# Performance work log

Hardware: AMD Instinct MI355X
Metric: run time of the kernel (lower is better)

## Reference

```python
import jax, jax.numpy as jnp
import numpy as np

NUM_HEADS = 12


def setup_inputs() -> dict:
    key = jax.random.key(0)
    ks = jax.random.split(key, 6)
    B, N, C = 16, 576, 768
    H, D = NUM_HEADS, 768 // NUM_HEADS
    P = 16
    x = jax.random.normal(ks[0], (B, N, C), dtype=jnp.float32)
    prompt = jax.random.normal(ks[1], (B, 2, P, H, D), dtype=jnp.float32)
    act_scale = jax.random.uniform(ks[2], (2,), dtype=jnp.float32)
    qkv_w = jax.random.normal(ks[3], (3 * C, C), dtype=jnp.float32) * (C ** -0.5)
    proj_w = jax.random.normal(ks[4], (C, C), dtype=jnp.float32) * (C ** -0.5)
    proj_b = jnp.zeros((C,), dtype=jnp.float32)
    return {"x": x, "prompt": prompt, "act_scale": act_scale,
            "qkv_w": qkv_w, "proj_w": proj_w, "proj_b": proj_b}


def reference(x, prompt, act_scale, qkv_w, proj_w, proj_b):
    B, N, C = x.shape
    H = NUM_HEADS
    D = C // H
    scale = D ** -0.5
    # qkv projection: [B,N,3C] -> (3,B,H,N,D)
    qkv = (x @ qkv_w.T).reshape(B, N, 3, H, D).transpose(2, 0, 3, 1, 4)
    q, k, v = qkv[0], qkv[1], qkv[2]
    # prompt: [B,2,P,H,D] -> (2,B,H,P,D)
    pr = jnp.transpose(prompt, (1, 0, 3, 2, 4))
    key_prefix, value_prefix = pr[0], pr[1]        # [B,H,P,D]
    v = jnp.concatenate([value_prefix, v], axis=2)  # [B,H,P+N,D]
    # gated prefix scores
    prompt_attn = jnp.einsum('bhnd,bhpd->bhnp', q, key_prefix) * scale
    prompt_attn = prompt_attn + jnp.tanh(prompt_attn * act_scale[0]) * act_scale[1]
    # standard scores
    attn = jnp.einsum('bhnd,bhmd->bhnm', q, k) * scale
    attn = jnp.concatenate([prompt_attn, attn], axis=-1)  # [B,H,N,P+N]
    attn = jax.nn.softmax(attn, axis=-1)
    out = jnp.einsum('bhnm,bhmd->bhnd', attn, v)  # [B,H,N,D]
    out = out.transpose(0, 2, 1, 3).reshape(B, N, C)
    return out @ proj_w.T + proj_b
```

## Files before the change

kernel.cpp:

```cpp
#include <hip/hip_runtime.h>
#include <hip/hip_bf16.h>
#include <math.h>

namespace {

constexpr int kB = 16, kN = 576, kC = 768, kH = 12, kP = 16;
constexpr int kM = kB * kN;

typedef __attribute__((ext_vector_type(8))) __bf16 bf16x8;
typedef __attribute__((ext_vector_type(4))) float  f32x4;
typedef __attribute__((ext_vector_type(8))) unsigned short u16x8;

__device__ inline unsigned short f2bf(float f) {
  __bf16 h = (__bf16)f;
  return __builtin_bit_cast(unsigned short, h);
}
__device__ inline float bf2f(unsigned short u) {
  unsigned int x = ((unsigned int)u) << 16;
  return __builtin_bit_cast(float, x);
}
__device__ inline unsigned int pk2bf(float lo, float hi) {
  return (unsigned int)f2bf(lo) | ((unsigned int)f2bf(hi) << 16);
}
__device__ inline int xcd_swz(int hw, int nwg) {
  const int per = nwg >> 3;
  return (hw & 7) * per + (hw >> 3);
}

#define GLDS16(src, dst) __builtin_amdgcn_global_load_lds( \
    (const __attribute__((address_space(1))) unsigned int*)(src), \
    (__attribute__((address_space(3))) unsigned int*)(dst), 16, 0, 0)

__global__ __launch_bounds__(256)
void cvt3(const float* __restrict__ x, const float* __restrict__ wq,
          const float* __restrict__ wp, unsigned short* __restrict__ xo,
          unsigned short* __restrict__ wqo, unsigned short* __restrict__ wpo) {
  const int bid = blockIdx.x;
  const float* in; unsigned short* out; int base;
  if (bid < 6912)       { in = x;  out = xo;  base = bid; }
  else if (bid < 8640)  { in = wq; out = wqo; base = bid - 6912; }
  else                  { in = wp; out = wpo; base = bid - 8640; }
  const int i = base * 256 + threadIdx.x;
  const float4 v = ((const float4*)in)[i];
  ((ushort4*)out)[i] = make_ushort4(f2bf(v.x), f2bf(v.y), f2bf(v.z), f2bf(v.w));
}

template<int OB>
__global__ __launch_bounds__(256)
void gemm_bf16(const unsigned short* __restrict__ A, const unsigned short* __restrict__ W,
               const float* __restrict__ bias, void* __restrict__ Yv, int Kd, int Nd) {
  __shared__ __align__(16) unsigned short As[2][4096];
  __shared__ __align__(16) unsigned short Bs[2][4096];
  const int tid  = threadIdx.x;
  const int wv   = tid >> 6, lane = tid & 63;
  const int gx   = Nd >> 7;
  const int lg   = xcd_swz(blockIdx.x, gridDim.x);
  const long bm  = (long)(lg / gx) * 128;
  const long bn  = (long)(lg % gx) * 128;
  const int wr   = (wv >> 1) * 64;
  const int wc   = (wv & 1) * 64;
  const int row15 = lane & 15, kg = lane >> 4;

  auto stage = [&](int buf, int kt) {
#pragma unroll
    for (int site = 0; site < 2; ++site) {
      const int p = site * 256 + tid;
      const int row = p >> 2, slot = (p & 3) ^ (row & 3);
      const unsigned short* srcA = A + (bm + row) * (long)Kd + kt + slot * 8;
      const unsigned short* srcB = W + (bn + row) * (long)Kd + kt + slot * 8;
      GLDS16(srcA, &As[buf][site * 2048 + wv * 512]);
      GLDS16(srcB, &Bs[buf][site * 2048 + wv * 512]);
    }
  };

  f32x4 acc[4][4] = {};
  stage(0, 0);
  __syncthreads();

  const int swg = row15 & 3;
  const int nt = Kd >> 5;
  for (int t = 0; t < nt; ++t) {
    const int cur = t & 1;
    if (t + 1 < nt) stage(cur ^ 1, (t + 1) << 5);

    bf16x8 af[4], bf_[4];
#pragma unroll
    for (int mi = 0; mi < 4; ++mi)
      af[mi] = *(const bf16x8*)(&As[cur][(wr + mi * 16 + row15) * 32 + ((kg ^ swg) << 3)]);
#pragma unroll
    for (int ni = 0; ni < 4; ++ni)
      bf_[ni] = *(const bf16x8*)(&Bs[cur][(wc + ni * 16 + row15) * 32 + ((kg ^ swg) << 3)]);
#pragma unroll
    for (int mi = 0; mi < 4; ++mi)
#pragma unroll
      for (int ni = 0; ni < 4; ++ni)
        acc[mi][ni] = __builtin_amdgcn_mfma_f32_16x16x32_bf16(af[mi], bf_[ni], acc[mi][ni], 0, 0, 0);
    __syncthreads();
  }

  const int r4 = kg * 4;
#pragma unroll
  for (int ni = 0; ni < 4; ++ni) {
    const long col = bn + wc + ni * 16 + row15;
    if constexpr (OB) {
      unsigned short* Y = (unsigned short*)Yv;
#pragma unroll
      for (int mi = 0; mi < 4; ++mi)
#pragma unroll
        for (int j = 0; j < 4; ++j)
          Y[(bm + wr + mi * 16 + r4 + j) * (long)Nd + col] = f2bf(acc[mi][ni][j]);
    } else {
      float* Y = (float*)Yv;
      const float bv = bias ? bias[col] : 0.0f;
#pragma unroll
      for (int mi = 0; mi < 4; ++mi)
#pragma unroll
        for (int j = 0; j < 4; ++j)
          Y[(bm + wr + mi * 16 + r4 + j) * (long)Nd + col] = acc[mi][ni][j] + bv;
    }
  }
}

__device__ inline void softmax_group_static(f32x4 (&c)[4], float& lsum,
                                            unsigned short* pl,
                                            const int kg, const int sw) {
  float psum = 0.0f;
#pragma unroll
  for (int kb = 0; kb < 4; ++kb) {
    const float p0 = __expf(c[kb][0] - 10.0f);
    const float p1 = __expf(c[kb][1] - 10.0f);
    const float p2 = __expf(c[kb][2] - 10.0f);
    const float p3 = __expf(c[kb][3] - 10.0f);
    psum += (p0 + p1) + (p2 + p3);
    const int off = (((kb * 2 + (kg >> 1)) ^ sw) << 3) + (kg & 1) * 4;
    *(uint2*)(pl + off) = make_uint2(pk2bf(p0, p1), pk2bf(p2, p3));
  }
  lsum += psum;
}

__global__ __launch_bounds__(192, 3)
void attn_mfma(const unsigned short* __restrict__ qkv, const float* __restrict__ prompt,
               const float* __restrict__ act_scale, unsigned short* __restrict__ attn_out) {
  const int lg = xcd_swz(blockIdx.x, gridDim.x);
  const int qt = lg % 6, bh = lg / 6;
  const int h = bh % kH, b = bh / kH;
  const int tid = threadIdx.x, wv = tid >> 6, lane = tid & 63;
  const int q15 = lane & 15, kg = lane >> 4;

  __shared__ __align__(16) unsigned short Klds[2][4096];
  __shared__ __align__(16) unsigned short Vt[2][4096];
  __shared__ __align__(16) unsigned short Plds[3][2048];

  const float a0 = act_scale[0], a1 = act_scale[1];
  const int sw  = q15 & 7;
  const int sl0 = (kg ^ sw) << 3;
  const int sl1 = ((4 + kg) ^ sw) << 3;

  bf16x8 qf[2][2];
#pragma unroll
  for (int g = 0; g < 2; ++g) {
    const unsigned short* qrow =
        qkv + (size_t)(b * kN + qt * 96 + wv * 32 + g * 16 + q15) * 2304 + h * 64;
#pragma unroll
    for (int dh = 0; dh < 2; ++dh) {
      u16x8 raw = *(const u16x8*)(qrow + dh * 32 + kg * 8);
      u16x8 sc;
#pragma unroll
      for (int j = 0; j < 8; ++j) sc[j] = f2bf(bf2f(raw[j]) * 0.125f);
      qf[g][dh] = __builtin_bit_cast(bf16x8, sc);
    }
  }

  if (tid < 128) {
    const int r = tid >> 3, s = tid & 7;
    const float* src = prompt + (((size_t)(b * 2) * kP + r) * kH + h) * 64 + s * 8;
    const f32x4 f0 = *(const f32x4*)src, f1 = *(const f32x4*)(src + 4);
    *(uint4*)(&Klds[0][r * 64 + ((s ^ (r & 7)) << 3)]) =
        make_uint4(pk2bf(f0[0], f0[1]), pk2bf(f0[2], f0[3]),
                   pk2bf(f1[0], f1[1]), pk2bf(f1[2], f1[3]));
  }
  if (tid < 128) {
    const int kp = tid & 7, vdq = tid >> 3;
    const float* s0 = prompt + (((size_t)(b * 2 + 1) * kP + 2 * kp) * kH + h) * 64 + vdq * 4;
    const f32x4 x0 = *(const f32x4*)s0;
    const f32x4 y0 = *(const f32x4*)(s0 + kH * 64);
#pragma unroll
    for (int j = 0; j < 4; ++j) {
      const int d = vdq * 4 + j;
      *(unsigned int*)(&Vt[0][d * 64 + (((kp >> 2) ^ (d & 7)) << 3) + (kp & 3) * 2]) =
          pk2bf(x0[j], y0[j]);
    }
  }
#pragma unroll
  for (int i = 0; i < 2; ++i) {
    const int idx = tid + 192 * i;
    const int d = idx / 6, szl = (idx % 6) + 2;
    *(uint4*)(&Vt[0][d * 64 + ((szl ^ (d & 7)) << 3)]) = make_uint4(0, 0, 0, 0);
  }
  __syncthreads();

  f32x4 o0[4] = {}, o1[4] = {};
  float l0 = 0.0f, l1 = 0.0f;

  const int vkp  = tid & 31;
  const int vdgb = tid >> 5;
  const int kr8  = lane >> 3, ks8 = lane & 7;

  for (int ch = 0; ch < 10; ++ch) {
    const int cur = ch & 1;

    u16x8 va0, va1, vb0, vb1;
    const bool doV = (ch < 9) && (wv < 2);
    if (ch < 9) {
      if (doV) {
        const unsigned short* r0 = qkv + (size_t)(b * kN + ch * 64 + 2 * vkp) * 2304 + 1536 + h * 64;
        va0 = *(const u16x8*)(r0 + vdgb * 8);
        va1 = *(const u16x8*)(r0 + (vdgb + 4) * 8);
        vb0 = *(const u16x8*)(r0 + 2304 + vdgb * 8);
        vb1 = *(const u16x8*)(r0 + 2304 + (vdgb + 4) * 8);
      } else if (wv == 2) {
#pragma unroll
        for (int g8 = 0; g8 < 8; ++g8) {
          const int r = g8 * 8 + kr8;
          const unsigned short* src =
              qkv + (size_t)(b * kN + ch * 64 + r) * 2304 + 768 + h * 64 + ((ks8 ^ (r & 7)) << 3);
          GLDS16(src, &Klds[cur ^ 1][g8 * 512]);
        }
      }
    }

    f32x4 c0[4], c1[4];
    __builtin_amdgcn_s_setprio(1);
#pragma unroll
    for (int kb = 0; kb < 4; ++kb) {
      if (ch == 0 && kb > 0) {
        c0[kb][0] = c0[kb][1] = c0[kb][2] = c0[kb][3] = -1.0e30f;
        c1[kb][0] = c1[kb][1] = c1[kb][2] = c1[kb][3] = -1.0e30f;
      } else {
        const unsigned short* krow = &Klds[cur][(kb * 16 + q15) * 64];
        const bf16x8 k0 = *(const bf16x8*)(krow + sl0);
        const bf16x8 k1 = *(const bf16x8*)(krow + sl1);
        f32x4 t0 = {}, t1 = {};
        t0 = __builtin_amdgcn_mfma_f32_16x16x32_bf16(k0, qf[0][0], t0, 0, 0, 0);
        c0[kb] = __builtin_amdgcn_mfma_f32_16x16x32_bf16(k1, qf[0][1], t0, 0, 0, 0);
        t1 = __builtin_amdgcn_mfma_f32_16x16x32_bf16(k0, qf[1][0], t1, 0, 0, 0);
        c1[kb] = __builtin_amdgcn_mfma_f32_16x16x32_bf16(k1, qf[1][1], t1, 0, 0, 0);
      }
    }
    __builtin_amdgcn_s_setprio(0);
    if (ch == 0) {
#pragma unroll
      for (int j = 0; j < 4; ++j) {
        const float s0v = c0[0][j];
        const float e0 = __expf(2.0f * s0v * a0);
        c0[0][j] = s0v + ((e0 - 1.0f) / (e0 + 1.0f)) * a1;
        const float s1v = c1[0][j];
        const float e1 = __expf(2.0f * s1v * a0);
        c1[0][j] = s1v + ((e1 - 1.0f) / (e1 + 1.0f)) * a1;
      }
    }

    softmax_group_static(c0, l0, &Plds[wv][q15 * 64], kg, sw);
    softmax_group_static(c1, l1, &Plds[wv][(q15 + 16) * 64], kg, sw);

    if (doV) {
#pragma unroll
      for (int j = 0; j < 8; ++j) {
        const int d0 = vdgb * 8 + j;
        *(unsigned int*)(&Vt[cur ^ 1][d0 * 64 + (((vkp >> 2) ^ (d0 & 7)) << 3) + (vkp & 3) * 2]) =
            (unsigned int)va0[j] | ((unsigned int)vb0[j] << 16);
        const int d1 = (vdgb + 4) * 8 + j;
        *(unsigned int*)(&Vt[cur ^ 1][d1 * 64 + (((vkp >> 2) ^ (d1 & 7)) << 3) + (vkp & 3) * 2]) =
            (unsigned int)va1[j] | ((unsigned int)vb1[j] << 16);
      }
    }

    const unsigned short* p0 = &Plds[wv][q15 * 64];
    const unsigned short* p1 = &Plds[wv][(q15 + 16) * 64];
    const bf16x8 pa00 = *(const bf16x8*)(p0 + sl0);
    const bf16x8 pa01 = *(const bf16x8*)(p0 + sl1);
    const bf16x8 pa10 = *(const bf16x8*)(p1 + sl0);
    const bf16x8 pa11 = *(const bf16x8*)(p1 + sl1);
    __builtin_amdgcn_s_setprio(1);
#pragma unroll
    for (int nb = 0; nb < 4; ++nb) {
      const unsigned short* vr = &Vt[cur][(nb * 16 + q15) * 64];
      const bf16x8 bv0 = *(const bf16x8*)(vr + sl0);
      const bf16x8 bv1 = *(const bf16x8*)(vr + sl1);
      o0[nb] = __builtin_amdgcn_mfma_f32_16x16x32_bf16(pa00, bv0, o0[nb], 0, 0, 0);
      o0[nb] = __builtin_amdgcn_mfma_f32_16x16x32_bf16(pa01, bv1, o0[nb], 0, 0, 0);
      o1[nb] = __builtin_amdgcn_mfma_f32_16x16x32_bf16(pa10, bv0, o1[nb], 0, 0, 0);
      o1[nb] = __builtin_amdgcn_mfma_f32_16x16x32_bf16(pa11, bv1, o1[nb], 0, 0, 0);
    }
    __builtin_amdgcn_s_setprio(0);

    __syncthreads();
  }

  l0 += __shfl_xor(l0, 16, 64);
  l0 += __shfl_xor(l0, 32, 64);
  l1 += __shfl_xor(l1, 16, 64);
  l1 += __shfl_xor(l1, 32, 64);
  const float i0 = 1.0f / l0, i1 = 1.0f / l1;
  float iq0[4], iq1[4];
#pragma unroll
  for (int jr = 0; jr < 4; ++jr) {
    iq0[jr] = __shfl(i0, kg * 4 + jr, 64);
    iq1[jr] = __shfl(i1, kg * 4 + jr, 64);
  }
  unsigned short* ob = attn_out + (size_t)(b * kN + qt * 96 + wv * 32) * 768 + h * 64;
#pragma unroll
  for (int nb = 0; nb < 4; ++nb)
#pragma unroll
    for (int jr = 0; jr < 4; ++jr) {
      ob[(size_t)(kg * 4 + jr) * 768 + nb * 16 + q15] = f2bf(o0[nb][jr] * iq0[jr]);
      ob[(size_t)(16 + kg * 4 + jr) * 768 + nb * 16 + q15] = f2bf(o1[nb][jr] * iq1[jr]);
    }
}

}

extern "C" void kernel_launch(void* const* d_in, const int* in_sizes, int n_in,
                              void* d_out, int out_size, void* d_ws, size_t ws_size,
                              hipStream_t stream) {
  const float* x         = (const float*)d_in[0];
  const float* prompt    = (const float*)d_in[1];
  const float* act_scale = (const float*)d_in[2];
  const float* qkv_w     = (const float*)d_in[3];
  const float* proj_w    = (const float*)d_in[4];
  const float* proj_b    = (const float*)d_in[5];
  float* out = (float*)d_out;

  char* ws = (char*)d_ws;
  unsigned short* qkvb   = (unsigned short*)ws;
  unsigned short* xa     = (unsigned short*)(ws + 42467328);
  unsigned short* qkvwb  = (unsigned short*)(ws + 42467328 + 14155776);
  unsigned short* projwb = (unsigned short*)(ws + 42467328 + 14155776 + 3538944);

  cvt3<<<9216, 256, 0, stream>>>(x, qkv_w, proj_w, xa, qkvwb, projwb);

  gemm_bf16<1><<<(3 * kC / 128) * (kM / 128), 256, 0, stream>>>(xa, qkvwb, nullptr, qkvb, kC, 3 * kC);
  attn_mfma<<<(kN / 96) * kH * kB, 192, 0, stream>>>(qkvb, prompt, act_scale, xa);
  gemm_bf16<0><<<(kC / 128) * (kM / 128), 256, 0, stream>>>(xa, projwb, proj_b, out, kC, kC);
}
```

Baseline: 125.5 us.

## Triple-buffer GEMM LDS staging with explicit vmcnt waits and raised MFMA priority

Moves the bf16 GEMM from double to triple buffering in LDS, prefetching two K-tiles ahead. It replaces __syncthreads with raw s_barrier plus explicit vmcnt waits so loads can stay in flight across iterations. It also raises wave priority around the MFMA block, removes the XOR swizzle on LDS reads and writes, and preloads the bias before the main loop. Dropping the swizzle risks LDS bank conflicts, and the extra buffer raises LDS use per block, which may lower occupancy.

```diff
diff --git a/kernel.cpp b/kernel.cpp
--- a/kernel.cpp
+++ b/kernel.cpp
@@ -49,8 +49,8 @@
 __global__ __launch_bounds__(256)
 void gemm_bf16(const unsigned short* __restrict__ A, const unsigned short* __restrict__ W,
                const float* __restrict__ bias, void* __restrict__ Yv, int Kd, int Nd) {
-  __shared__ __align__(16) unsigned short As[2][4096];
-  __shared__ __align__(16) unsigned short Bs[2][4096];
+  __shared__ __align__(16) unsigned short As[3][4096];
+  __shared__ __align__(16) unsigned short Bs[3][4096];
   const int tid  = threadIdx.x;
   const int wv   = tid >> 6, lane = tid & 63;
   const int gx   = Nd >> 7;
@@ -65,37 +65,50 @@
 #pragma unroll
     for (int site = 0; site < 2; ++site) {
       const int p = site * 256 + tid;
-      const int row = p >> 2, slot = (p & 3) ^ (row & 3);
-      const unsigned short* srcA = A + (bm + row) * (long)Kd + kt + slot * 8;
-      const unsigned short* srcB = W + (bn + row) * (long)Kd + kt + slot * 8;
+      const unsigned short* srcA = A + (bm + (p >> 2)) * (long)Kd + kt + (p & 3) * 8;
+      const unsigned short* srcB = W + (bn + (p >> 2)) * (long)Kd + kt + (p & 3) * 8;
       GLDS16(srcA, &As[buf][site * 2048 + wv * 512]);
       GLDS16(srcB, &Bs[buf][site * 2048 + wv * 512]);
     }
   };
 
+  float bvpre[4] = {0.0f, 0.0f, 0.0f, 0.0f};
+  if constexpr (!OB) {
+#pragma unroll
+    for (int ni = 0; ni < 4; ++ni) bvpre[ni] = bias[bn + wc + ni * 16 + row15];
+  }
+  asm volatile("s_waitcnt vmcnt(0)" ::: "memory");
+
   f32x4 acc[4][4] = {};
   stage(0, 0);
-  __syncthreads();
-
-  const int swg = row15 & 3;
+  stage(1, 32);
+
   const int nt = Kd >> 5;
   for (int t = 0; t < nt; ++t) {
-    const int cur = t & 1;
-    if (t + 1 < nt) stage(cur ^ 1, (t + 1) << 5);
+    const int cur = t % 3;
+    __builtin_amdgcn_sched_barrier(0);
+    __builtin_amdgcn_s_barrier();
+    if (t + 2 < nt) stage((t + 2) % 3, (t + 2) << 5);
+    if (t + 2 < nt)      asm volatile("s_waitcnt vmcnt(8)");
+    else if (t + 1 < nt) asm volatile("s_waitcnt vmcnt(4)");
+    else                 asm volatile("s_waitcnt vmcnt(0)");
+    __builtin_amdgcn_s_barrier();
+    __builtin_amdgcn_sched_barrier(0);
 
     bf16x8 af[4], bf_[4];
 #pragma unroll
     for (int mi = 0; mi < 4; ++mi)
-      af[mi] = *(const bf16x8*)(&As[cur][(wr + mi * 16 + row15) * 32 + ((kg ^ swg) << 3)]);
+      af[mi] = *(const bf16x8*)(&As[cur][(wr + mi * 16 + row15) * 32 + kg * 8]);
 #pragma unroll
     for (int ni = 0; ni < 4; ++ni)
-      bf_[ni] = *(const bf16x8*)(&Bs[cur][(wc + ni * 16 + row15) * 32 + ((kg ^ swg) << 3)]);
+      bf_[ni] = *(const bf16x8*)(&Bs[cur][(wc + ni * 16 + row15) * 32 + kg * 8]);
+    __builtin_amdgcn_s_setprio(1);
 #pragma unroll
     for (int mi = 0; mi < 4; ++mi)
 #pragma unroll
       for (int ni = 0; ni < 4; ++ni)
         acc[mi][ni] = __builtin_amdgcn_mfma_f32_16x16x32_bf16(af[mi], bf_[ni], acc[mi][ni], 0, 0, 0);
-    __syncthreads();
+    __builtin_amdgcn_s_setprio(0);
   }
 
   const int r4 = kg * 4;
@@ -111,12 +124,11 @@
           Y[(bm + wr + mi * 16 + r4 + j) * (long)Nd + col] = f2bf(acc[mi][ni][j]);
     } else {
       float* Y = (float*)Yv;
-      const float bv = bias ? bias[col] : 0.0f;
 #pragma unroll
       for (int mi = 0; mi < 4; ++mi)
 #pragma unroll
         for (int j = 0; j < 4; ++j)
-          Y[(bm + wr + mi * 16 + r4 + j) * (long)Nd + col] = acc[mi][ni][j] + bv;
+          Y[(bm + wr + mi * 16 + r4 + j) * (long)Nd + col] = acc[mi][ni][j] + bvpre[ni];
     }
   }
 }
```

Measured after the change: 124.3 us. Within noise of the previous version (-0.9%).
